# Optimization experiments

Measured on AMD Instinct MI355X. Metric: run time of the kernel, lower is better.

Reference implementation:

```python
import jax, jax.numpy as jnp
import numpy as np

N, NC, E, S = 65536, 24576, 524288, 256
VAR_DIM, H1, H2, H3, H4 = 6, 128, 128, 256, 128
THRE, EPS = 0.7, 1e-5


def _bn(x, g, b):
    # BatchNorm1d, training-mode batch statistics (biased var), dropout treated as identity
    mu = x.mean(0)
    v = x.var(0)
    return (x - mu) * jax.lax.rsqrt(v + EPS) * g + b


def _gcn_sparse(h, src, dst, ew, W, b):
    # PyG GCNConv with edge weights: add self-loops (weight 1), symmetric normalization
    n = h.shape[0]
    loop = jnp.arange(n)
    s = jnp.concatenate([src, loop])
    d = jnp.concatenate([dst, loop])
    w = jnp.concatenate([ew, jnp.ones((n,), h.dtype)])
    deg = jax.ops.segment_sum(w, d, num_segments=n)
    dinv = jnp.where(deg > 0, jax.lax.rsqrt(deg), 0.0)
    norm = dinv[s] * w * dinv[d]
    xw = h @ W.T  # [n, out]
    out = jax.ops.segment_sum(norm[:, None] * xw[s], d, num_segments=n)
    return out + b


def _gcn_dense(h, A, W, b):
    # GCNConv on a dense binary adjacency (no edge weights), self-loops + sym norm
    n = h.shape[0]
    A_hat = A + jnp.eye(n, dtype=h.dtype)
    deg = A_hat.sum(0)
    dinv = jnp.where(deg > 0, jax.lax.rsqrt(deg), 0.0)
    return dinv[:, None] * (A_hat.T @ ((h @ W.T) * dinv[:, None])) + b


def setup_inputs() -> dict:
    key = jax.random.key(0)
    ks = jax.random.split(key, 10)

    def w(k, o, i):
        return jax.random.normal(k, (o, i), jnp.float32) / np.float32(np.sqrt(i))

    x = jax.random.normal(ks[0], (N, VAR_DIM), jnp.float32)
    edge_attr = jax.random.uniform(ks[1], (E,), jnp.float32)
    scen_adj = jax.random.uniform(ks[2], (S, S), jnp.float32)
    edge_index = jax.random.randint(ks[3], (2, E), 0, N)
    batch = jnp.arange(N) // (N // S)  # sorted node->graph ids, 256 nodes per graph
    mark = jnp.concatenate([jnp.ones((NC,), jnp.int32), jnp.zeros((N - NC,), jnp.int32)])
    return {
        "x": x, "edge_attr": edge_attr, "scen_adj": scen_adj,
        "mlp_var_w": w(ks[4], H1, VAR_DIM), "mlp_var_b": jnp.zeros((H1,), jnp.float32),
        "mlp_con_w": w(ks[5], H1, 1), "mlp_con_b": jnp.zeros((H1,), jnp.float32),
        "conv1_w": w(ks[6], H2, H1), "conv1_b": jnp.zeros((H2,), jnp.float32),
        "conv2_w": w(ks[7], H3, H2), "conv2_b": jnp.zeros((H3,), jnp.float32),
        "conv3_w": w(ks[8], H4, H3), "conv3_b": jnp.zeros((H4,), jnp.float32),
        "bn1_g": jnp.ones((H1,), jnp.float32), "bn1_b": jnp.zeros((H1,), jnp.float32),
        "bn2_g": jnp.ones((H2,), jnp.float32), "bn2_b": jnp.zeros((H2,), jnp.float32),
        "bn3_g": jnp.ones((H3,), jnp.float32), "bn3_b": jnp.zeros((H3,), jnp.float32),
        "mark": mark, "edge_index": edge_index, "batch": batch, "n_con": NC,
    }


def reference(x, edge_attr, scen_adj, mlp_var_w, mlp_var_b, mlp_con_w, mlp_con_b,
              conv1_w, conv1_b, conv2_w, conv2_b, conv3_w, conv3_b,
              bn1_g, bn1_b, bn2_g, bn2_b, bn3_g, bn3_b,
              mark, edge_index, batch, n_con):
    nc = int(n_con)  # mark layout: first nc nodes are constraints (mark==1), rest vars
    con_feat = jnp.tanh(x[:nc, 0:1] @ mlp_con_w.T + mlp_con_b)
    var_feat = jnp.tanh(x[nc:] @ mlp_var_w.T + mlp_var_b)
    h = jnp.concatenate([con_feat, var_feat], axis=0)  # [N, H1], con-first as in torch cat
    h = _bn(h, bn1_g, bn1_b)  # dropout = identity (eval)
    h = _gcn_sparse(h, edge_index[0], edge_index[1], edge_attr, conv1_w, conv1_b)
    h = jnp.tanh(_bn(h, bn2_g, bn2_b))
    s = scen_adj.shape[0]
    sums = jax.ops.segment_sum(h, batch, num_segments=s)
    cnt = jax.ops.segment_sum(jnp.ones((h.shape[0],), h.dtype), batch, num_segments=s)
    pooled = sums / jnp.maximum(cnt, 1.0)[:, None]  # global_mean_pool -> [S, H2]
    A = (scen_adj >= THRE).astype(h.dtype)  # filter_adj + unweighted edges
    f = jnp.tanh(_bn(_gcn_dense(pooled, A, conv2_w, conv2_b), bn3_g, bn3_b))
    feat = jnp.tanh(_gcn_dense(f, A, conv3_w, conv3_b))
    return feat, feat.mean(0)
```

## Files before the change

kernel.cpp:

```cpp
#include <hip/hip_runtime.h>
#include <hip/hip_bf16.h>
#include <cstddef>

#define N_NODES 65536
#define N_EDGES 524288
#define S_GRAPH 256
#define BN_EPS 1e-5f
#define THRE 0.7f

typedef __hip_bfloat16 bf16;
typedef unsigned int uint32;
typedef unsigned char uchar;
typedef unsigned short ushort16;
typedef __attribute__((ext_vector_type(8))) short short8;
typedef __attribute__((ext_vector_type(4))) float f32x4;

__device__ __forceinline__ float blo(uint32 u) { return __uint_as_float(u << 16); }
__device__ __forceinline__ float bhi(uint32 u) { return __uint_as_float(u & 0xffff0000u); }

__device__ __forceinline__ uint32 packbf(float a, float b)
{
    bf16 ha = __float2bfloat16(a), hb = __float2bfloat16(b);
    unsigned short ua, ub;
    __builtin_memcpy(&ua, &ha, 2); __builtin_memcpy(&ub, &hb, 2);
    return (uint32)ua | ((uint32)ub << 16);
}

__device__ __forceinline__ float ftanh(float x)
{
    float e = __builtin_amdgcn_exp2f(x * 2.8853900817779268f);
    return 1.0f - 2.0f * __builtin_amdgcn_rcpf(e + 1.0f);
}

__global__ __launch_bounds__(256) void k_mlp_hist(
    const float* __restrict__ x, const float* __restrict__ wv,
    const float* __restrict__ bv, const float* __restrict__ wc,
    const float* __restrict__ bc, const int* __restrict__ nconp,
    uint32* __restrict__ h0u, float* __restrict__ stats,
    const int* __restrict__ dst, uint32* __restrict__ blkhist,
    const float* __restrict__ scen, float* __restrict__ fcol,
    const float* __restrict__ w1f, uint32* __restrict__ w1bk)
{
    __shared__ float xs[128 * 6];
    __shared__ float sh[256];
    __shared__ uint32 bh[256];
    int t = threadIdx.x;
    int b = blockIdx.x;
    if (b < 512) {
        bh[t] = 0;
        __syncthreads();
        int e0 = b * 1024 + t * 4;
        int4 d4 = *(const int4*)(dst + e0);
        atomicAdd(&bh[d4.x >> 8], 1u);
        atomicAdd(&bh[d4.y >> 8], 1u);
        atomicAdd(&bh[d4.z >> 8], 1u);
        atomicAdd(&bh[d4.w >> 8], 1u);
        __syncthreads();
        blkhist[b * 256 + t] = bh[t];
        return;
    }
    if (b >= 1024) {
        if (b < 1056) {
            int r0 = (b - 1024) * 8;
            float s = 0.f;
            for (int r = r0; r < r0 + 8; r++)
                s += (scen[r * 256 + t] >= THRE) ? 1.0f : 0.0f;
            atomicAdd(&fcol[t], s);
        } else {
            const float4* w4 = (const float4*)w1f;
            uint2* wo = (uint2*)w1bk;
            #pragma unroll
            for (int it = 0; it < 16; it++) {
                int fi = it * 256 + t;
                float4 w = w4[fi];
                wo[fi] = make_uint2(packbf(w.x, w.y), packbf(w.z, w.w));
            }
        }
        return;
    }
    int n0 = (b - 512) * 128;
    if (t < 192) ((float4*)xs)[t] = ((const float4*)(x + (size_t)n0 * 6))[t];
    __syncthreads();

    int nc = *nconp;
    int lane = t & 63, wave = t >> 6;
    int j0 = 2 * lane;
    const float2* wv2 = (const float2*)wv;
    float2 wa0 = wv2[j0 * 3], wa1 = wv2[j0 * 3 + 1], wa2 = wv2[j0 * 3 + 2];
    float2 wb0 = wv2[j0 * 3 + 3], wb1 = wv2[j0 * 3 + 4], wb2 = wv2[j0 * 3 + 5];
    float wc0 = wc[j0], wc1 = wc[j0 + 1], bc0 = bc[j0], bc1 = bc[j0 + 1];
    float bv0 = bv[j0], bv1 = bv[j0 + 1];

    float s0 = 0.f, ss0 = 0.f, s1 = 0.f, ss1 = 0.f;
    #pragma unroll 4
    for (int m = 0; m < 32; m++) {
        int ln = wave * 32 + m;
        int n = n0 + ln;
        const float* xr = &xs[ln * 6];
        float a0, a1;
        if (n < nc) {
            float xv = xr[0];
            a0 = xv * wc0 + bc0; a1 = xv * wc1 + bc1;
        } else {
            float x0 = xr[0], x1 = xr[1], x2 = xr[2], x3 = xr[3], x4 = xr[4], x5 = xr[5];
            a0 = bv0 + x0 * wa0.x + x1 * wa0.y + x2 * wa1.x + x3 * wa1.y + x4 * wa2.x + x5 * wa2.y;
            a1 = bv1 + x0 * wb0.x + x1 * wb0.y + x2 * wb1.x + x3 * wb1.y + x4 * wb2.x + x5 * wb2.y;
        }
        uint32 pk = packbf(ftanh(a0), ftanh(a1));
        h0u[(size_t)n * 64 + lane] = pk;
        float v0 = blo(pk), v1 = bhi(pk);
        s0 += v0; ss0 += v0 * v0; s1 += v1; ss1 += v1 * v1;
    }
    sh[t] = s0; __syncthreads();
    if (t < 64) atomicAdd(&stats[2 * t], sh[t] + sh[t + 64] + sh[t + 128] + sh[t + 192]);
    __syncthreads(); sh[t] = s1; __syncthreads();
    if (t < 64) atomicAdd(&stats[2 * t + 1], sh[t] + sh[t + 64] + sh[t + 128] + sh[t + 192]);
    __syncthreads(); sh[t] = ss0; __syncthreads();
    if (t < 64) atomicAdd(&stats[128 + 2 * t], sh[t] + sh[t + 64] + sh[t + 128] + sh[t + 192]);
    __syncthreads(); sh[t] = ss1; __syncthreads();
    if (t < 64) atomicAdd(&stats[128 + 2 * t + 1], sh[t] + sh[t + 64] + sh[t + 128] + sh[t + 192]);
}

__global__ __launch_bounds__(256) void k_binscan(
    const uint32* __restrict__ blkhist, uint32* __restrict__ blkoff,
    uint32* __restrict__ binsz, uint32* __restrict__ ubase,
    uint32* __restrict__ pbase, int* __restrict__ ctr)
{
    __shared__ uint32 v[512];
    __shared__ uint32 ps[256];
    __shared__ int flag;
    int g = blockIdx.x, t = threadIdx.x;
    v[t]       = blkhist[t * 256 + g];
    v[t + 256] = blkhist[(t + 256) * 256 + g];
    __syncthreads();
    uint32 a0 = v[2 * t], a1 = v[2 * t + 1];
    ps[t] = a0 + a1; __syncthreads();
    for (int o = 1; o < 256; o <<= 1) {
        uint32 u = (t >= o) ? ps[t - o] : 0;
        __syncthreads();
        ps[t] += u;
        __syncthreads();
    }
    uint32 ex = ps[t] - (a0 + a1);
    ((uint2*)blkoff)[g * 256 + t] = make_uint2(ex, ex + a0);
    if (t == 255) atomicExch((int*)&binsz[g], (int)ps[255]);
    __syncthreads();
    if (t == 0) {
        __threadfence();
        flag = (atomicAdd(ctr, 1) == 255) ? 1 : 0;
    }
    __syncthreads();
    if (flag) {
        __threadfence();
        uint32 s = binsz[t];
        ps[t] = s; __syncthreads();
        for (int o = 1; o < 256; o <<= 1) {
            uint32 u = (t >= o) ? ps[t - o] : 0;
            __syncthreads();
            ps[t] += u;
            __syncthreads();
        }
        ubase[t] = ps[t] - s;
        pbase[t] = ps[t] - s + (uint32)t * 768u;
    }
}

__global__ __launch_bounds__(256) void k_scatter(
    const int* __restrict__ src, const int* __restrict__ dst,
    const float* __restrict__ ew, const uint32* __restrict__ blkoff,
    const uint32* __restrict__ ubase, uint2* __restrict__ ebin)
{
    __shared__ uint32 bh[256];
    __shared__ uint32 bo[256];
    int b = blockIdx.x, t = threadIdx.x;
    bh[t] = 0;
    bo[t] = ubase[t] + blkoff[t * 512 + b];
    __syncthreads();
    int e0 = b * 1024 + t * 4;
    int4 d4 = *(const int4*)(dst + e0);
    int4 s4 = *(const int4*)(src + e0);
    float4 w4 = *(const float4*)(ew + e0);
    int bin; uint32 r;
    bin = d4.x >> 8; r = atomicAdd(&bh[bin], 1u);
    ebin[bo[bin] + r] = make_uint2((uint32)s4.x | ((uint32)(d4.x & 255) << 16), __float_as_uint(w4.x));
    bin = d4.y >> 8; r = atomicAdd(&bh[bin], 1u);
    ebin[bo[bin] + r] = make_uint2((uint32)s4.y | ((uint32)(d4.y & 255) << 16), __float_as_uint(w4.y));
    bin = d4.z >> 8; r = atomicAdd(&bh[bin], 1u);
    ebin[bo[bin] + r] = make_uint2((uint32)s4.z | ((uint32)(d4.z & 255) << 16), __float_as_uint(w4.z));
    bin = d4.w >> 8; r = atomicAdd(&bh[bin], 1u);
    ebin[bo[bin] + r] = make_uint2((uint32)s4.w | ((uint32)(d4.w & 255) << 16), __float_as_uint(w4.w));
}

__global__ __launch_bounds__(256) void k_csr(
    const uint2* __restrict__ ebin, const uint32* __restrict__ binsz,
    const uint32* __restrict__ ubase, const uint32* __restrict__ pbase,
    float* __restrict__ dinv, int* __restrict__ rowp, int* __restrict__ cnts,
    int2* __restrict__ epk)
{
    __shared__ uint2 es[3072];
    __shared__ uint32 hist[256];
    __shared__ int sscan[256];
    __shared__ int rloc[256];
    __shared__ float dlv[256];
    int g = blockIdx.x, t = threadIdx.x;
    int start = (int)ubase[g];
    int sz = min((int)binsz[g], 3072);
    int pb = (int)pbase[g];
    hist[t] = 0;
    __syncthreads();
    for (int i = t; i < sz; i += 256) {
        uint2 e = ebin[start + i];
        int dl = (e.x >> 16) & 255;
        uint32 wfix = __float2uint_rn(__uint_as_float(e.y) * 262144.0f);
        uint32 h = atomicAdd(&hist[dl], (1u << 24) | wfix);
        e.x |= (h >> 24) << 24;
        es[i] = e;
    }
    __syncthreads();
    uint32 hv = hist[t];
    int cnt = (int)(hv >> 24);
    float di = rsqrtf((float)(hv & 0xFFFFFFu) * 3.814697265625e-6f + 1.0f);
    dlv[t] = di;
    dinv[g * 256 + t] = di;
    cnts[g * 256 + t] = cnt;
    int pcnt = (cnt + 3) & ~3;
    sscan[t] = pcnt; __syncthreads();
    for (int o = 1; o < 256; o <<= 1) {
        int u = (t >= o) ? sscan[t - o] : 0;
        __syncthreads();
        sscan[t] += u;
        __syncthreads();
    }
    int rl = sscan[t] - pcnt;
    rloc[t] = rl;
    rowp[g * 256 + t] = pb + rl;
    __syncthreads();
    for (int i = t; i < sz; i += 256) {
        uint2 e = es[i];
        int s  = (int)(e.x & 0xFFFFu);
        int dl = (int)((e.x >> 16) & 255u);
        int r  = (int)(e.x >> 24);
        float w = __uint_as_float(e.y) * dlv[dl];
        epk[pb + rloc[dl] + r] = make_int2(s, __float_as_int(w));
    }
    int base = pb + rl;
    for (int q = cnt; q < pcnt; q++) epk[base + q] = make_int2(g * 256 + t, 0);
}

__global__ __launch_bounds__(256) void k_gemm1f(
    const uint32* __restrict__ h0u, const uint32* __restrict__ w1bk,
    const float* __restrict__ g1, const float* __restrict__ bb1,
    const float* __restrict__ stats, ushort16* __restrict__ xws,
    const float* __restrict__ dinv)
{
    __shared__ short hn_s[64 * 136];
    __shared__ short w_s[128 * 136];
    __shared__ float sc[128], sf[128];
    int t = threadIdx.x;
    int blk = blockIdx.x;
    int row0 = blk * 64;

    if (t < 128) {
        float mu  = stats[t] * (1.0f / N_NODES);
        float var = stats[128 + t] * (1.0f / N_NODES) - mu * mu;
        float rs  = rsqrtf(fmaxf(var, 0.f) + BN_EPS);
        float s   = rs * g1[t];
        sc[t] = s;
        sf[t] = bb1[t] - mu * s;
    }
    __syncthreads();

    const uint4* h4 = (const uint4*)(h0u + (size_t)row0 * 64);
    #pragma unroll
    for (int it = 0; it < 4; it++) {
        int slot = it * 256 + t;
        int r = slot >> 4, k0 = (slot & 15) * 8;
        uint4 u = h4[slot];
        uint32 ua[4] = {u.x, u.y, u.z, u.w};
        uint32 o[4];
        #pragma unroll
        for (int m = 0; m < 4; m++) {
            int k = k0 + 2 * m;
            o[m] = packbf(blo(ua[m]) * sc[k] + sf[k], bhi(ua[m]) * sc[k + 1] + sf[k + 1]);
        }
        *(uint4*)&hn_s[r * 136 + k0] = make_uint4(o[0], o[1], o[2], o[3]);
    }
    const uint4* wv4 = (const uint4*)w1bk;
    #pragma unroll
    for (int it = 0; it < 8; it++) {
        int s2 = it * 256 + t;
        int c = s2 >> 4, k0 = (s2 & 15) * 8;
        *(uint4*)&w_s[c * 136 + k0] = wv4[s2];
    }
    __syncthreads();

    int lane = t & 63, wave = t >> 6;
    int m16 = lane & 15, kh = lane >> 4;
    int mbase = wave * 16;
    f32x4 acc[8] = {};
    #pragma unroll
    for (int ks = 0; ks < 4; ks++) {
        short8 a = *(const short8*)&hn_s[(mbase + m16) * 136 + ks * 32 + kh * 8];
        #pragma unroll
        for (int ct = 0; ct < 8; ct++) {
            short8 bfr = *(const short8*)&w_s[(ct * 16 + m16) * 136 + ks * 32 + kh * 8];
            acc[ct] = __builtin_amdgcn_mfma_f32_16x16x32_bf16(a, bfr, acc[ct], 0, 0, 0);
        }
    }
    float dvr[4];
    #pragma unroll
    for (int r = 0; r < 4; r++) dvr[r] = dinv[row0 + mbase + kh * 4 + r];
    #pragma unroll
    for (int ct = 0; ct < 8; ct++) {
        int col = ct * 16 + m16;
        #pragma unroll
        for (int r = 0; r < 4; r++) {
            int row = mbase + kh * 4 + r;
            bf16 hv = __float2bfloat16(acc[ct][r] * dvr[r]);
            unsigned short us; __builtin_memcpy(&us, &hv, 2);
            xws[(size_t)(row0 + row) * 128 + col] = us;
        }
    }
}

__global__ __launch_bounds__(256) void k_gather(
    const int* __restrict__ rowp, const int* __restrict__ cnts,
    const int2* __restrict__ epk, const uint32* __restrict__ xwu,
    const float* __restrict__ dinv, const float2* __restrict__ b1c2,
    uint32* __restrict__ aggu, float* __restrict__ stats2r)
{
    __shared__ float sh[256];
    int t = threadIdx.x, b = blockIdx.x;
    int lane = t & 63, wave = t >> 6;
    float2 bb = b1c2[lane];
    float s0 = 0.f, ss0 = 0.f, s1 = 0.f, ss1 = 0.f;
    for (int it = 0; it < 8; it++) {
        int n = b * 32 + it * 4 + wave;
        int st = rowp[n];
        int pcnt = (cnts[n] + 3) & ~3;
        float di = dinv[n];
        uint32 u0 = xwu[(size_t)n * 64 + lane];
        float ax = di * blo(u0) + bb.x;
        float ay = di * bhi(u0) + bb.y;
        int en = st + pcnt;
        for (int p = st; p < en; p += 4) {
            int2 q0 = epk[p], q1 = epk[p + 1], q2 = epk[p + 2], q3 = epk[p + 3];
            uint32 v0 = xwu[(size_t)q0.x * 64 + lane];
            uint32 v1 = xwu[(size_t)q1.x * 64 + lane];
            uint32 v2 = xwu[(size_t)q2.x * 64 + lane];
            uint32 v3 = xwu[(size_t)q3.x * 64 + lane];
            float w0 = __int_as_float(q0.y), w1 = __int_as_float(q1.y);
            float w2 = __int_as_float(q2.y), w3 = __int_as_float(q3.y);
            ax += w0 * blo(v0) + w1 * blo(v1) + w2 * blo(v2) + w3 * blo(v3);
            ay += w0 * bhi(v0) + w1 * bhi(v1) + w2 * bhi(v2) + w3 * bhi(v3);
        }
        uint32 pk = packbf(ax, ay);
        aggu[(size_t)n * 64 + lane] = pk;
        float v0 = blo(pk), v1 = bhi(pk);
        s0 += v0; ss0 += v0 * v0; s1 += v1; ss1 += v1 * v1;
    }
    float* st2 = stats2r + (b & 7) * 256;
    sh[t] = s0; __syncthreads();
    if (t < 64) atomicAdd(&st2[2 * t], sh[t] + sh[t + 64] + sh[t + 128] + sh[t + 192]);
    __syncthreads(); sh[t] = s1; __syncthreads();
    if (t < 64) atomicAdd(&st2[2 * t + 1], sh[t] + sh[t + 64] + sh[t + 128] + sh[t + 192]);
    __syncthreads(); sh[t] = ss0; __syncthreads();
    if (t < 64) atomicAdd(&st2[128 + 2 * t], sh[t] + sh[t + 64] + sh[t + 128] + sh[t + 192]);
    __syncthreads(); sh[t] = ss1; __syncthreads();
    if (t < 64) atomicAdd(&st2[128 + 2 * t + 1], sh[t] + sh[t + 64] + sh[t + 128] + sh[t + 192]);
}

__global__ __launch_bounds__(512) void k_poolg2(
    const uint32* __restrict__ aggu, const float* __restrict__ stats2r,
    const float* __restrict__ g2, const float* __restrict__ bb2,
    const float* __restrict__ w2, float* __restrict__ z1)
{
    __shared__ float sc[128], sf[128], sh[512], prow[128];
    int t = threadIdx.x, g = blockIdx.x;
    if (t < 128) {
        float su = 0.f, sq = 0.f;
        #pragma unroll
        for (int r = 0; r < 8; r++) {
            su += stats2r[r * 256 + t];
            sq += stats2r[r * 256 + 128 + t];
        }
        float mu  = su * (1.0f / N_NODES);
        float var = sq * (1.0f / N_NODES) - mu * mu;
        float rs  = rsqrtf(fmaxf(var, 0.f) + BN_EPS);
        float s   = rs * g2[t];
        sc[t] = s;
        sf[t] = bb2[t] - mu * s;
    }
    __syncthreads();
    int c = t & 63, grp = t >> 6;
    float c0s = sc[2 * c], c0f = sf[2 * c], c1s = sc[2 * c + 1], c1f = sf[2 * c + 1];
    const uint32* base = aggu + (size_t)g * 256 * 64;
    float s0 = 0.f, s1 = 0.f;
    for (int r = grp * 32; r < grp * 32 + 32; r++) {
        uint32 u = base[r * 64 + c];
        s0 += ftanh(blo(u) * c0s + c0f);
        s1 += ftanh(bhi(u) * c1s + c1f);
    }
    sh[t] = s0; __syncthreads();
    if (t < 64) {
        float acc = 0.f;
        #pragma unroll
        for (int k = 0; k < 8; k++) acc += sh[t + 64 * k];
        prow[2 * t] = acc * (1.0f / 256.0f);
    }
    __syncthreads(); sh[t] = s1; __syncthreads();
    if (t < 64) {
        float acc = 0.f;
        #pragma unroll
        for (int k = 0; k < 8; k++) acc += sh[t + 64 * k];
        prow[2 * t + 1] = acc * (1.0f / 256.0f);
    }
    __syncthreads();
    if (t < 256) {
        float acc = 0.f;
        const float* wr = w2 + t * 128;
        for (int k = 0; k < 128; k++) acc += prow[k] * wr[k];
        z1[g * 256 + t] = acc;
    }
}

__global__ void k_dgcn1(const float* __restrict__ scen, const float* __restrict__ fcol,
                        const float* __restrict__ z1, const float* __restrict__ b2c,
                        float* __restrict__ y1, float* __restrict__ stats3r)
{
    __shared__ float wk[256];
    int i = blockIdx.x, t = threadIdx.x;
    float a = (scen[t * 256 + i] >= THRE) ? 1.0f : 0.0f;
    if (t == i) a += 1.0f;
    wk[t] = a * rsqrtf(fcol[t] + 1.0f);
    __syncthreads();
    float acc = 0.f;
    for (int k = 0; k < 256; k++) acc += wk[k] * z1[k * 256 + t];
    float v = rsqrtf(fcol[i] + 1.0f) * acc + b2c[t];
    y1[i * 256 + t] = v;
    float* s3 = stats3r + (i & 7) * 512;
    atomicAdd(&s3[t], v);
    atomicAdd(&s3[256 + t], v * v);
}

__global__ void k_gemm3(const float* __restrict__ y1, const float* __restrict__ stats3r,
                        const float* __restrict__ g3, const float* __restrict__ bb3,
                        const float* __restrict__ w3, float* __restrict__ z2)
{
    __shared__ float row[256];
    int i = blockIdx.x, t = threadIdx.x;
    for (int c = t; c < 256; c += 128) {
        float s = 0.f, ss = 0.f;
        #pragma unroll
        for (int r = 0; r < 8; r++) {
            s  += stats3r[r * 512 + c];
            ss += stats3r[r * 512 + 256 + c];
        }
        float mu  = s * (1.0f / 256.0f);
        float var = ss * (1.0f / 256.0f) - mu * mu;
        float rs  = rsqrtf(fmaxf(var, 0.f) + BN_EPS);
        float scj = rs * g3[c];
        float sfj = bb3[c] - mu * scj;
        row[c] = ftanh(y1[i * 256 + c] * scj + sfj);
    }
    __syncthreads();
    float acc = 0.f;
    const float* wr = w3 + t * 256;
    for (int k = 0; k < 256; k++) acc += row[k] * wr[k];
    z2[i * 128 + t] = acc;
}

__global__ void k_dgcn2(const float* __restrict__ scen, const float* __restrict__ fcol,
                        const float* __restrict__ z2, const float* __restrict__ b3c,
                        float* __restrict__ out, float* __restrict__ meanr,
                        int* __restrict__ ctr)
{
    __shared__ float wk[256];
    __shared__ int flag;
    int i = blockIdx.x, t = threadIdx.x;
    for (int k = t; k < 256; k += 128) {
        float a = (scen[k * 256 + i] >= THRE) ? 1.0f : 0.0f;
        if (k == i) a += 1.0f;
        wk[k] = a * rsqrtf(fcol[k] + 1.0f);
    }
    __syncthreads();
    float acc = 0.f;
    for (int k = 0; k < 256; k++) acc += wk[k] * z2[k * 128 + t];
    float v = ftanh(rsqrtf(fcol[i] + 1.0f) * acc + b3c[t]);
    out[i * 128 + t] = v;
    atomicAdd(&meanr[(i & 7) * 128 + t], v);
    __syncthreads();
    if (t == 0) {
        __threadfence();
        flag = (atomicAdd(ctr, 1) == 255) ? 1 : 0;
    }
    __syncthreads();
    if (flag) {
        __threadfence();
        float s = 0.f;
        #pragma unroll
        for (int r = 0; r < 8; r++) s += meanr[r * 128 + t];
        out[S_GRAPH * 128 + t] = s * (1.0f / 256.0f);
    }
}

extern "C" void kernel_launch(void* const* d_in, const int* in_sizes, int n_in,
                              void* d_out, int out_size, void* d_ws, size_t ws_size,
                              hipStream_t stream)
{
    const float* x        = (const float*)d_in[0];
    const float* edge_attr= (const float*)d_in[1];
    const float* scen     = (const float*)d_in[2];
    const float* wv       = (const float*)d_in[3];
    const float* bv       = (const float*)d_in[4];
    const float* wc       = (const float*)d_in[5];
    const float* bc       = (const float*)d_in[6];
    const float* w1       = (const float*)d_in[7];
    const float* b1c      = (const float*)d_in[8];
    const float* w2       = (const float*)d_in[9];
    const float* b2c      = (const float*)d_in[10];
    const float* w3       = (const float*)d_in[11];
    const float* b3c      = (const float*)d_in[12];
    const float* g1       = (const float*)d_in[13];
    const float* bb1      = (const float*)d_in[14];
    const float* g2       = (const float*)d_in[15];
    const float* bb2      = (const float*)d_in[16];
    const float* g3       = (const float*)d_in[17];
    const float* bb3      = (const float*)d_in[18];
    const int*  ei        = (const int*)d_in[20];
    const int*  nconp     = (const int*)d_in[22];
    const int*  src = ei;
    const int*  dst = ei + N_EDGES;

    float* wsf = (float*)d_ws;
    uint32*   h0u  = (uint32*)wsf;
    uint32*   aggu = (uint32*)wsf;
    uint32*   xwu  = (uint32*)(wsf + 4194304);
    float* zb      = wsf + 8388608;
    float* stats1  = zb;
    float* stats2r = zb + 512;
    float* stats3r = zb + 2560;
    float* fcol    = zb + 6656;
    float* meanr   = zb + 6912;
    int*   ctrs    = (int*)(zb + 7936);
    const int ZN   = 7944;
    float* deg     = zb + ZN;
    int*   rowp    = (int*)(deg + 65536);
    int*   cnts    = rowp + 65536;
    uint32* blkhist= (uint32*)(cnts + 65536);
    uint32* blkoff = blkhist + 131072;
    uint32* binsz  = blkoff + 131072;
    uint32* ubase  = binsz + 256;
    uint32* pbase  = ubase + 256;
    uint2* ebin    = (uint2*)(pbase + 256);
    int2*  epk     = (int2*)(ebin + 524288);
    uint32* w1bk   = (uint32*)(epk + 720896);
    float* z1      = (float*)(w1bk + 8192);
    float* y1      = z1 + 65536;
    float* z2      = y1 + 65536;

    float* out = (float*)d_out;

    hipMemsetAsync(zb, 0, ZN * sizeof(float), stream);

    k_mlp_hist<<<1057, 256, 0, stream>>>(x, wv, bv, wc, bc, nconp, h0u, stats1,
                                         dst, blkhist, scen, fcol, w1, w1bk);
    k_binscan<<<256, 256, 0, stream>>>(blkhist, blkoff, binsz, ubase, pbase, &ctrs[0]);
    k_scatter<<<512, 256, 0, stream>>>(src, dst, edge_attr, blkoff, ubase, ebin);
    k_csr<<<256, 256, 0, stream>>>(ebin, binsz, ubase, pbase, deg, rowp, cnts, epk);
    k_gemm1f<<<1024, 256, 0, stream>>>(h0u, w1bk, g1, bb1, stats1, (ushort16*)xwu, deg);
    k_gather<<<2048, 256, 0, stream>>>(rowp, cnts, epk, xwu, deg,
                                       (const float2*)b1c, aggu, stats2r);
    k_poolg2<<<S_GRAPH, 512, 0, stream>>>(aggu, stats2r, g2, bb2, w2, z1);
    k_dgcn1<<<256, 256, 0, stream>>>(scen, fcol, z1, b2c, y1, stats3r);
    k_gemm3<<<256, 128, 0, stream>>>(y1, stats3r, g3, bb3, w3, z2);
    k_dgcn2<<<256, 128, 0, stream>>>(scen, fcol, z2, b3c, out, meanr, &ctrs[1]);
}
```

Measured before the change: 253.3 us.

## Fuse front-end and tail kernels into persistent kernels with grid barriers

Merges the MLP/histogram, bin scan, scatter and CSR-build kernels into one 1057-block kernel separated by software grid barriers. It also merges the four small dense-GCN tail kernels into one 256-block kernel. The aim is to remove kernel launch gaps and drain/ramp overhead between many short dependent stages. The cost is that the grid barriers require every block to be co-resident, which is why launch bounds were raised to 5 blocks per CU. Barrier spin and a larger shared-memory footprint could also reduce occupancy.

```diff
diff --git a/kernel.cpp b/kernel.cpp
--- a/kernel.cpp
+++ b/kernel.cpp
@@ -32,21 +32,43 @@
     return 1.0f - 2.0f * __builtin_amdgcn_rcpf(e + 1.0f);
 }
 
-__global__ __launch_bounds__(256) void k_mlp_hist(
+__device__ __forceinline__ void gbar(int* bar, int nblk)
+{
+    __syncthreads();
+    if (threadIdx.x == 0) {
+        __builtin_amdgcn_fence(__ATOMIC_RELEASE, "agent");
+        int gen = __hip_atomic_load(bar + 1, __ATOMIC_RELAXED, __HIP_MEMORY_SCOPE_AGENT);
+        if (__hip_atomic_fetch_add(bar, 1, __ATOMIC_RELAXED, __HIP_MEMORY_SCOPE_AGENT) == nblk - 1) {
+            __hip_atomic_store(bar, 0, __ATOMIC_RELAXED, __HIP_MEMORY_SCOPE_AGENT);
+            __hip_atomic_fetch_add(bar + 1, 1, __ATOMIC_RELAXED, __HIP_MEMORY_SCOPE_AGENT);
+        } else {
+            while (__hip_atomic_load(bar + 1, __ATOMIC_RELAXED, __HIP_MEMORY_SCOPE_AGENT) == gen)
+                __builtin_amdgcn_s_sleep(8);
+        }
+        __builtin_amdgcn_fence(__ATOMIC_ACQUIRE, "agent");
+    }
+    __syncthreads();
+}
+
+__global__ __launch_bounds__(256, 5) void k_front(
     const float* __restrict__ x, const float* __restrict__ wv,
     const float* __restrict__ bv, const float* __restrict__ wc,
     const float* __restrict__ bc, const int* __restrict__ nconp,
     uint32* __restrict__ h0u, float* __restrict__ stats,
-    const int* __restrict__ dst, uint32* __restrict__ blkhist,
+    const int* __restrict__ src, const int* __restrict__ dst,
+    const float* __restrict__ ew, uint32* __restrict__ blkhist,
+    uint32* __restrict__ blkoff, uint32* __restrict__ binsz,
     const float* __restrict__ scen, float* __restrict__ fcol,
-    const float* __restrict__ w1f, uint32* __restrict__ w1bk)
-{
-    __shared__ float xs[128 * 6];
-    __shared__ float sh[256];
-    __shared__ uint32 bh[256];
+    const float* __restrict__ w1f, uint32* __restrict__ w1bk,
+    float* __restrict__ dinv, int* __restrict__ rowp, int* __restrict__ cnts,
+    uint2* __restrict__ ebin, int2* __restrict__ epk, int* __restrict__ bar)
+{
+    __shared__ __align__(16) uchar smem[29696];
     int t = threadIdx.x;
     int b = blockIdx.x;
+
     if (b < 512) {
+        uint32* bh = (uint32*)smem;
         bh[t] = 0;
         __syncthreads();
         int e0 = b * 1024 + t * 4;
@@ -57,101 +79,93 @@
         atomicAdd(&bh[d4.w >> 8], 1u);
         __syncthreads();
         blkhist[b * 256 + t] = bh[t];
-        return;
-    }
-    if (b >= 1024) {
-        if (b < 1056) {
-            int r0 = (b - 1024) * 8;
-            float s = 0.f;
-            for (int r = r0; r < r0 + 8; r++)
-                s += (scen[r * 256 + t] >= THRE) ? 1.0f : 0.0f;
-            atomicAdd(&fcol[t], s);
-        } else {
-            const float4* w4 = (const float4*)w1f;
-            uint2* wo = (uint2*)w1bk;
-            #pragma unroll
-            for (int it = 0; it < 16; it++) {
-                int fi = it * 256 + t;
-                float4 w = w4[fi];
-                wo[fi] = make_uint2(packbf(w.x, w.y), packbf(w.z, w.w));
+    } else if (b < 1024) {
+        float* xs = (float*)smem;
+        float* sh = (float*)(smem + 3072);
+        int n0 = (b - 512) * 128;
+        if (t < 192) ((float4*)xs)[t] = ((const float4*)(x + (size_t)n0 * 6))[t];
+        __syncthreads();
+
+        int nc = *nconp;
+        int lane = t & 63, wave = t >> 6;
+        int j0 = 2 * lane;
+        const float2* wv2 = (const float2*)wv;
+        float2 wa0 = wv2[j0 * 3], wa1 = wv2[j0 * 3 + 1], wa2 = wv2[j0 * 3 + 2];
+        float2 wb0 = wv2[j0 * 3 + 3], wb1 = wv2[j0 * 3 + 4], wb2 = wv2[j0 * 3 + 5];
+        float wc0 = wc[j0], wc1 = wc[j0 + 1], bc0 = bc[j0], bc1 = bc[j0 + 1];
+        float bv0 = bv[j0], bv1 = bv[j0 + 1];
+
+        float s0 = 0.f, ss0 = 0.f, s1 = 0.f, ss1 = 0.f;
+        #pragma unroll 4
+        for (int m = 0; m < 32; m++) {
+            int ln = wave * 32 + m;
+            int n = n0 + ln;
+            const float* xr = &xs[ln * 6];
+            float a0, a1;
+            if (n < nc) {
+                float xv = xr[0];
+                a0 = xv * wc0 + bc0; a1 = xv * wc1 + bc1;
+            } else {
+                float x0 = xr[0], x1 = xr[1], x2 = xr[2], x3 = xr[3], x4 = xr[4], x5 = xr[5];
+                a0 = bv0 + x0 * wa0.x + x1 * wa0.y + x2 * wa1.x + x3 * wa1.y + x4 * wa2.x + x5 * wa2.y;
+                a1 = bv1 + x0 * wb0.x + x1 * wb0.y + x2 * wb1.x + x3 * wb1.y + x4 * wb2.x + x5 * wb2.y;
             }
-        }
-        return;
-    }
-    int n0 = (b - 512) * 128;
-    if (t < 192) ((float4*)xs)[t] = ((const float4*)(x + (size_t)n0 * 6))[t];
-    __syncthreads();
-
-    int nc = *nconp;
-    int lane = t & 63, wave = t >> 6;
-    int j0 = 2 * lane;
-    const float2* wv2 = (const float2*)wv;
-    float2 wa0 = wv2[j0 * 3], wa1 = wv2[j0 * 3 + 1], wa2 = wv2[j0 * 3 + 2];
-    float2 wb0 = wv2[j0 * 3 + 3], wb1 = wv2[j0 * 3 + 4], wb2 = wv2[j0 * 3 + 5];
-    float wc0 = wc[j0], wc1 = wc[j0 + 1], bc0 = bc[j0], bc1 = bc[j0 + 1];
-    float bv0 = bv[j0], bv1 = bv[j0 + 1];
-
-    float s0 = 0.f, ss0 = 0.f, s1 = 0.f, ss1 = 0.f;
-    #pragma unroll 4
-    for (int m = 0; m < 32; m++) {
-        int ln = wave * 32 + m;
-        int n = n0 + ln;
-        const float* xr = &xs[ln * 6];
-        float a0, a1;
-        if (n < nc) {
-            float xv = xr[0];
-            a0 = xv * wc0 + bc0; a1 = xv * wc1 + bc1;
-        } else {
-            float x0 = xr[0], x1 = xr[1], x2 = xr[2], x3 = xr[3], x4 = xr[4], x5 = xr[5];
-            a0 = bv0 + x0 * wa0.x + x1 * wa0.y + x2 * wa1.x + x3 * wa1.y + x4 * wa2.x + x5 * wa2.y;
-            a1 = bv1 + x0 * wb0.x + x1 * wb0.y + x2 * wb1.x + x3 * wb1.y + x4 * wb2.x + x5 * wb2.y;
-        }
-        uint32 pk = packbf(ftanh(a0), ftanh(a1));
-        h0u[(size_t)n * 64 + lane] = pk;
-        float v0 = blo(pk), v1 = bhi(pk);
-        s0 += v0; ss0 += v0 * v0; s1 += v1; ss1 += v1 * v1;
-    }
-    sh[t] = s0; __syncthreads();
-    if (t < 64) atomicAdd(&stats[2 * t], sh[t] + sh[t + 64] + sh[t + 128] + sh[t + 192]);
-    __syncthreads(); sh[t] = s1; __syncthreads();
-    if (t < 64) atomicAdd(&stats[2 * t + 1], sh[t] + sh[t + 64] + sh[t + 128] + sh[t + 192]);
-    __syncthreads(); sh[t] = ss0; __syncthreads();
-    if (t < 64) atomicAdd(&stats[128 + 2 * t], sh[t] + sh[t + 64] + sh[t + 128] + sh[t + 192]);
-    __syncthreads(); sh[t] = ss1; __syncthreads();
-    if (t < 64) atomicAdd(&stats[128 + 2 * t + 1], sh[t] + sh[t + 64] + sh[t + 128] + sh[t + 192]);
-}
-
-__global__ __launch_bounds__(256) void k_binscan(
-    const uint32* __restrict__ blkhist, uint32* __restrict__ blkoff,
-    uint32* __restrict__ binsz, uint32* __restrict__ ubase,
-    uint32* __restrict__ pbase, int* __restrict__ ctr)
-{
-    __shared__ uint32 v[512];
-    __shared__ uint32 ps[256];
-    __shared__ int flag;
-    int g = blockIdx.x, t = threadIdx.x;
-    v[t]       = blkhist[t * 256 + g];
-    v[t + 256] = blkhist[(t + 256) * 256 + g];
-    __syncthreads();
-    uint32 a0 = v[2 * t], a1 = v[2 * t + 1];
-    ps[t] = a0 + a1; __syncthreads();
-    for (int o = 1; o < 256; o <<= 1) {
-        uint32 u = (t >= o) ? ps[t - o] : 0;
-        __syncthreads();
-        ps[t] += u;
-        __syncthreads();
-    }
-    uint32 ex = ps[t] - (a0 + a1);
-    ((uint2*)blkoff)[g * 256 + t] = make_uint2(ex, ex + a0);
-    if (t == 255) atomicExch((int*)&binsz[g], (int)ps[255]);
-    __syncthreads();
-    if (t == 0) {
-        __threadfence();
-        flag = (atomicAdd(ctr, 1) == 255) ? 1 : 0;
-    }
-    __syncthreads();
-    if (flag) {
-        __threadfence();
+            uint32 pk = packbf(ftanh(a0), ftanh(a1));
+            h0u[(size_t)n * 64 + lane] = pk;
+            float v0 = blo(pk), v1 = bhi(pk);
+            s0 += v0; ss0 += v0 * v0; s1 += v1; ss1 += v1 * v1;
+        }
+        sh[t] = s0; __syncthreads();
+        if (t < 64) atomicAdd(&stats[2 * t], sh[t] + sh[t + 64] + sh[t + 128] + sh[t + 192]);
+        __syncthreads(); sh[t] = s1; __syncthreads();
+        if (t < 64) atomicAdd(&stats[2 * t + 1], sh[t] + sh[t + 64] + sh[t + 128] + sh[t + 192]);
+        __syncthreads(); sh[t] = ss0; __syncthreads();
+        if (t < 64) atomicAdd(&stats[128 + 2 * t], sh[t] + sh[t + 64] + sh[t + 128] + sh[t + 192]);
+        __syncthreads(); sh[t] = ss1; __syncthreads();
+        if (t < 64) atomicAdd(&stats[128 + 2 * t + 1], sh[t] + sh[t + 64] + sh[t + 128] + sh[t + 192]);
+    } else if (b < 1056) {
+        int r0 = (b - 1024) * 8;
+        float s = 0.f;
+        for (int r = r0; r < r0 + 8; r++)
+            s += (scen[r * 256 + t] >= THRE) ? 1.0f : 0.0f;
+        atomicAdd(&fcol[t], s);
+    } else {
+        const float4* w4 = (const float4*)w1f;
+        uint2* wo = (uint2*)w1bk;
+        #pragma unroll
+        for (int it = 0; it < 16; it++) {
+            int fi = it * 256 + t;
+            float4 w = w4[fi];
+            wo[fi] = make_uint2(packbf(w.x, w.y), packbf(w.z, w.w));
+        }
+    }
+    gbar(bar, 1057);
+
+    if (b < 256) {
+        uint32* v  = (uint32*)smem;
+        uint32* ps = (uint32*)(smem + 2048);
+        int g = b;
+        v[t]       = blkhist[t * 256 + g];
+        v[t + 256] = blkhist[(t + 256) * 256 + g];
+        __syncthreads();
+        uint32 a0 = v[2 * t], a1 = v[2 * t + 1];
+        ps[t] = a0 + a1; __syncthreads();
+        for (int o = 1; o < 256; o <<= 1) {
+            uint32 u = (t >= o) ? ps[t - o] : 0;
+            __syncthreads();
+            ps[t] += u;
+            __syncthreads();
+        }
+        uint32 ex = ps[t] - (a0 + a1);
+        ((uint2*)blkoff)[g * 256 + t] = make_uint2(ex, ex + a0);
+        if (t == 255) binsz[g] = ps[255];
+    }
+    gbar(bar, 1057);
+
+    if (b < 512) {
+        uint32* ps = (uint32*)smem;
+        uint32* bo = (uint32*)(smem + 1024);
+        uint32* bh = (uint32*)(smem + 2048);
         uint32 s = binsz[t];
         ps[t] = s; __syncthreads();
         for (int o = 1; o < 256; o <<= 1) {
@@ -160,91 +174,88 @@
             ps[t] += u;
             __syncthreads();
         }
-        ubase[t] = ps[t] - s;
-        pbase[t] = ps[t] - s + (uint32)t * 768u;
-    }
-}
-
-__global__ __launch_bounds__(256) void k_scatter(
-    const int* __restrict__ src, const int* __restrict__ dst,
-    const float* __restrict__ ew, const uint32* __restrict__ blkoff,
-    const uint32* __restrict__ ubase, uint2* __restrict__ ebin)
-{
-    __shared__ uint32 bh[256];
-    __shared__ uint32 bo[256];
-    int b = blockIdx.x, t = threadIdx.x;
-    bh[t] = 0;
-    bo[t] = ubase[t] + blkoff[t * 512 + b];
-    __syncthreads();
-    int e0 = b * 1024 + t * 4;
-    int4 d4 = *(const int4*)(dst + e0);
-    int4 s4 = *(const int4*)(src + e0);
-    float4 w4 = *(const float4*)(ew + e0);
-    int bin; uint32 r;
-    bin = d4.x >> 8; r = atomicAdd(&bh[bin], 1u);
-    ebin[bo[bin] + r] = make_uint2((uint32)s4.x | ((uint32)(d4.x & 255) << 16), __float_as_uint(w4.x));
-    bin = d4.y >> 8; r = atomicAdd(&bh[bin], 1u);
-    ebin[bo[bin] + r] = make_uint2((uint32)s4.y | ((uint32)(d4.y & 255) << 16), __float_as_uint(w4.y));
-    bin = d4.z >> 8; r = atomicAdd(&bh[bin], 1u);
-    ebin[bo[bin] + r] = make_uint2((uint32)s4.z | ((uint32)(d4.z & 255) << 16), __float_as_uint(w4.z));
-    bin = d4.w >> 8; r = atomicAdd(&bh[bin], 1u);
-    ebin[bo[bin] + r] = make_uint2((uint32)s4.w | ((uint32)(d4.w & 255) << 16), __float_as_uint(w4.w));
-}
-
-__global__ __launch_bounds__(256) void k_csr(
-    const uint2* __restrict__ ebin, const uint32* __restrict__ binsz,
-    const uint32* __restrict__ ubase, const uint32* __restrict__ pbase,
-    float* __restrict__ dinv, int* __restrict__ rowp, int* __restrict__ cnts,
-    int2* __restrict__ epk)
-{
-    __shared__ uint2 es[3072];
-    __shared__ uint32 hist[256];
-    __shared__ int sscan[256];
-    __shared__ int rloc[256];
-    __shared__ float dlv[256];
-    int g = blockIdx.x, t = threadIdx.x;
-    int start = (int)ubase[g];
-    int sz = min((int)binsz[g], 3072);
-    int pb = (int)pbase[g];
-    hist[t] = 0;
-    __syncthreads();
-    for (int i = t; i < sz; i += 256) {
-        uint2 e = ebin[start + i];
-        int dl = (e.x >> 16) & 255;
-        uint32 wfix = __float2uint_rn(__uint_as_float(e.y) * 262144.0f);
-        uint32 h = atomicAdd(&hist[dl], (1u << 24) | wfix);
-        e.x |= (h >> 24) << 24;
-        es[i] = e;
-    }
-    __syncthreads();
-    uint32 hv = hist[t];
-    int cnt = (int)(hv >> 24);
-    float di = rsqrtf((float)(hv & 0xFFFFFFu) * 3.814697265625e-6f + 1.0f);
-    dlv[t] = di;
-    dinv[g * 256 + t] = di;
-    cnts[g * 256 + t] = cnt;
-    int pcnt = (cnt + 3) & ~3;
-    sscan[t] = pcnt; __syncthreads();
-    for (int o = 1; o < 256; o <<= 1) {
-        int u = (t >= o) ? sscan[t - o] : 0;
-        __syncthreads();
-        sscan[t] += u;
-        __syncthreads();
-    }
-    int rl = sscan[t] - pcnt;
-    rloc[t] = rl;
-    rowp[g * 256 + t] = pb + rl;
-    __syncthreads();
-    for (int i = t; i < sz; i += 256) {
-        uint2 e = es[i];
-        int s  = (int)(e.x & 0xFFFFu);
-        int dl = (int)((e.x >> 16) & 255u);
-        int r  = (int)(e.x >> 24);
-        float w = __uint_as_float(e.y) * dlv[dl];
-        epk[pb + rloc[dl] + r] = make_int2(s, __float_as_int(w));
-    }
-    int base = pb + rl;
-    for (int q = cnt; q < pcnt; q++) epk[base + q] = make_int2(g * 256 + t, 0);
+        bo[t] = (ps[t] - s) + blkoff[t * 512 + b];
+        bh[t] = 0;
+        __syncthreads();
+        int e0 = b * 1024 + t * 4;
+        int4 d4 = *(const int4*)(dst + e0);
+        int4 s4 = *(const int4*)(src + e0);
+        float4 w4 = *(const float4*)(ew + e0);
+        int bin; uint32 r;
+        bin = d4.x >> 8; r = atomicAdd(&bh[bin], 1u);
+        ebin[bo[bin] + r] = make_uint2((uint32)s4.x | ((uint32)(d4.x & 255) << 16), __float_as_uint(w4.x));
+        bin = d4.y >> 8; r = atomicAdd(&bh[bin], 1u);
+        ebin[bo[bin] + r] = make_uint2((uint32)s4.y | ((uint32)(d4.y & 255) << 16), __float_as_uint(w4.y));
+        bin = d4.z >> 8; r = atomicAdd(&bh[bin], 1u);
+        ebin[bo[bin] + r] = make_uint2((uint32)s4.z | ((uint32)(d4.z & 255) << 16), __float_as_uint(w4.z));
+        bin = d4.w >> 8; r = atomicAdd(&bh[bin], 1u);
+        ebin[bo[bin] + r] = make_uint2((uint32)s4.w | ((uint32)(d4.w & 255) << 16), __float_as_uint(w4.w));
+    }
+    gbar(bar, 1057);
+
+    if (b < 256) {
+        uint2* es    = (uint2*)smem;
+        uint32* hist = (uint32*)(smem + 24576);
+        int* sscan   = (int*)(smem + 25600);
+        int* rloc    = (int*)(smem + 26624);
+        float* dlv   = (float*)(smem + 27648);
+        uint32* ubl  = (uint32*)(smem + 28672);
+        int g = b;
+        {
+            uint32 s = binsz[t];
+            sscan[t] = (int)s; __syncthreads();
+            for (int o = 1; o < 256; o <<= 1) {
+                int u = (t >= o) ? sscan[t - o] : 0;
+                __syncthreads();
+                sscan[t] += u;
+                __syncthreads();
+            }
+            ubl[t] = (uint32)sscan[t] - s;
+        }
+        __syncthreads();
+        int start = (int)ubl[g];
+        int sz = min((int)binsz[g], 3072);
+        int pb = start + g * 768;
+        hist[t] = 0;
+        __syncthreads();
+        for (int i2 = t; i2 < sz; i2 += 256) {
+            uint2 e = ebin[start + i2];
+            int dl = (e.x >> 16) & 255;
+            uint32 wfix = __float2uint_rn(__uint_as_float(e.y) * 262144.0f);
+            uint32 h = atomicAdd(&hist[dl], (1u << 24) | wfix);
+            e.x |= (h >> 24) << 24;
+            es[i2] = e;
+        }
+        __syncthreads();
+        uint32 hv = hist[t];
+        int cnt = (int)(hv >> 24);
+        float di = rsqrtf((float)(hv & 0xFFFFFFu) * 3.814697265625e-6f + 1.0f);
+        dlv[t] = di;
+        dinv[g * 256 + t] = di;
+        cnts[g * 256 + t] = cnt;
+        int pcnt = (cnt + 3) & ~3;
+        sscan[t] = pcnt; __syncthreads();
+        for (int o = 1; o < 256; o <<= 1) {
+            int u = (t >= o) ? sscan[t - o] : 0;
+            __syncthreads();
+            sscan[t] += u;
+            __syncthreads();
+        }
+        int rl = sscan[t] - pcnt;
+        rloc[t] = rl;
+        rowp[g * 256 + t] = pb + rl;
+        __syncthreads();
+        for (int i2 = t; i2 < sz; i2 += 256) {
+            uint2 e = es[i2];
+            int s2 = (int)(e.x & 0xFFFFu);
+            int dl = (int)((e.x >> 16) & 255u);
+            int r  = (int)(e.x >> 24);
+            float w = __uint_as_float(e.y) * dlv[dl];
+            epk[pb + rloc[dl] + r] = make_int2(s2, __float_as_int(w));
+        }
+        int basep = pb + rl;
+        for (int q = cnt; q < pcnt; q++) epk[basep + q] = make_int2(g * 256 + t, 0);
+    }
 }
 
 __global__ __launch_bounds__(256) void k_gemm1f(
@@ -370,137 +381,146 @@
     if (t < 64) atomicAdd(&st2[128 + 2 * t + 1], sh[t] + sh[t + 64] + sh[t + 128] + sh[t + 192]);
 }
 
-__global__ __launch_bounds__(512) void k_poolg2(
+__global__ __launch_bounds__(256) void k_tail(
     const uint32* __restrict__ aggu, const float* __restrict__ stats2r,
     const float* __restrict__ g2, const float* __restrict__ bb2,
-    const float* __restrict__ w2, float* __restrict__ z1)
-{
-    __shared__ float sc[128], sf[128], sh[512], prow[128];
-    int t = threadIdx.x, g = blockIdx.x;
-    if (t < 128) {
-        float su = 0.f, sq = 0.f;
-        #pragma unroll
-        for (int r = 0; r < 8; r++) {
-            su += stats2r[r * 256 + t];
-            sq += stats2r[r * 256 + 128 + t];
-        }
-        float mu  = su * (1.0f / N_NODES);
-        float var = sq * (1.0f / N_NODES) - mu * mu;
-        float rs  = rsqrtf(fmaxf(var, 0.f) + BN_EPS);
-        float s   = rs * g2[t];
-        sc[t] = s;
-        sf[t] = bb2[t] - mu * s;
-    }
-    __syncthreads();
-    int c = t & 63, grp = t >> 6;
-    float c0s = sc[2 * c], c0f = sf[2 * c], c1s = sc[2 * c + 1], c1f = sf[2 * c + 1];
-    const uint32* base = aggu + (size_t)g * 256 * 64;
-    float s0 = 0.f, s1 = 0.f;
-    for (int r = grp * 32; r < grp * 32 + 32; r++) {
-        uint32 u = base[r * 64 + c];
-        s0 += ftanh(blo(u) * c0s + c0f);
-        s1 += ftanh(bhi(u) * c1s + c1f);
-    }
-    sh[t] = s0; __syncthreads();
-    if (t < 64) {
+    const float* __restrict__ w2, float* __restrict__ z1,
+    const float* __restrict__ scen, const float* __restrict__ fcol,
+    const float* __restrict__ b2c, float* __restrict__ y1,
+    float* __restrict__ stats3r, const float* __restrict__ g3,
+    const float* __restrict__ bb3, const float* __restrict__ w3,
+    float* __restrict__ z2, const float* __restrict__ b3c,
+    float* __restrict__ out, float* __restrict__ meanr,
+    int* __restrict__ ctr, int* __restrict__ bar)
+{
+    __shared__ __align__(16) uchar smem[2560];
+    __shared__ int flagP10;
+    int t = threadIdx.x;
+    int b = blockIdx.x;
+
+    {
+        float* sc   = (float*)smem;
+        float* sf   = (float*)(smem + 512);
+        float* sh   = (float*)(smem + 1024);
+        float* prow = (float*)(smem + 2048);
+        int g = b;
+        if (t < 128) {
+            float su = 0.f, sq = 0.f;
+            #pragma unroll
+            for (int r = 0; r < 8; r++) {
+                su += stats2r[r * 256 + t];
+                sq += stats2r[r * 256 + 128 + t];
+            }
+            float mu  = su * (1.0f / N_NODES);
+            float var = sq * (1.0f / N_NODES) - mu * mu;
+            float rs  = rsqrtf(fmaxf(var, 0.f) + BN_EPS);
+            float s   = rs * g2[t];
+            sc[t] = s;
+            sf[t] = bb2[t] - mu * s;
+        }
+        __syncthreads();
+        int c = t & 63, grp = t >> 6;
+        float c0s = sc[2 * c], c0f = sf[2 * c], c1s = sc[2 * c + 1], c1f = sf[2 * c + 1];
+        const uint32* base = aggu + (size_t)g * 256 * 64;
+        float s0 = 0.f, s1 = 0.f;
+        for (int r = grp * 64; r < grp * 64 + 64; r++) {
+            uint32 u = base[r * 64 + c];
+            s0 += ftanh(blo(u) * c0s + c0f);
+            s1 += ftanh(bhi(u) * c1s + c1f);
+        }
+        sh[t] = s0; __syncthreads();
+        if (t < 64) {
+            float acc = sh[t] + sh[t + 64] + sh[t + 128] + sh[t + 192];
+            prow[2 * t] = acc * (1.0f / 256.0f);
+        }
+        __syncthreads(); sh[t] = s1; __syncthreads();
+        if (t < 64) {
+            float acc = sh[t] + sh[t + 64] + sh[t + 128] + sh[t + 192];
+            prow[2 * t + 1] = acc * (1.0f / 256.0f);
+        }
+        __syncthreads();
+        float accv = 0.f;
+        const float* wr = w2 + t * 128;
+        for (int k = 0; k < 128; k++) accv += prow[k] * wr[k];
+        z1[g * 256 + t] = accv;
+    }
+    gbar(bar, 256);
+
+    {
+        float* wk = (float*)smem;
+        int i = b;
+        float aa = (scen[t * 256 + i] >= THRE) ? 1.0f : 0.0f;
+        if (t == i) aa += 1.0f;
+        wk[t] = aa * rsqrtf(fcol[t] + 1.0f);
+        __syncthreads();
         float acc = 0.f;
-        #pragma unroll
-        for (int k = 0; k < 8; k++) acc += sh[t + 64 * k];
-        prow[2 * t] = acc * (1.0f / 256.0f);
-    }
-    __syncthreads(); sh[t] = s1; __syncthreads();
-    if (t < 64) {
-        float acc = 0.f;
-        #pragma unroll
-        for (int k = 0; k < 8; k++) acc += sh[t + 64 * k];
-        prow[2 * t + 1] = acc * (1.0f / 256.0f);
-    }
-    __syncthreads();
-    if (t < 256) {
-        float acc = 0.f;
-        const float* wr = w2 + t * 128;
-        for (int k = 0; k < 128; k++) acc += prow[k] * wr[k];
-        z1[g * 256 + t] = acc;
-    }
-}
-
-__global__ void k_dgcn1(const float* __restrict__ scen, const float* __restrict__ fcol,
-                        const float* __restrict__ z1, const float* __restrict__ b2c,
-                        float* __restrict__ y1, float* __restrict__ stats3r)
-{
-    __shared__ float wk[256];
-    int i = blockIdx.x, t = threadIdx.x;
-    float a = (scen[t * 256 + i] >= THRE) ? 1.0f : 0.0f;
-    if (t == i) a += 1.0f;
-    wk[t] = a * rsqrtf(fcol[t] + 1.0f);
-    __syncthreads();
-    float acc = 0.f;
-    for (int k = 0; k < 256; k++) acc += wk[k] * z1[k * 256 + t];
-    float v = rsqrtf(fcol[i] + 1.0f) * acc + b2c[t];
-    y1[i * 256 + t] = v;
-    float* s3 = stats3r + (i & 7) * 512;
-    atomicAdd(&s3[t], v);
-    atomicAdd(&s3[256 + t], v * v);
-}
-
-__global__ void k_gemm3(const float* __restrict__ y1, const float* __restrict__ stats3r,
-                        const float* __restrict__ g3, const float* __restrict__ bb3,
-                        const float* __restrict__ w3, float* __restrict__ z2)
-{
-    __shared__ float row[256];
-    int i = blockIdx.x, t = threadIdx.x;
-    for (int c = t; c < 256; c += 128) {
-        float s = 0.f, ss = 0.f;
-        #pragma unroll
-        for (int r = 0; r < 8; r++) {
-            s  += stats3r[r * 512 + c];
-            ss += stats3r[r * 512 + 256 + c];
-        }
-        float mu  = s * (1.0f / 256.0f);
-        float var = ss * (1.0f / 256.0f) - mu * mu;
-        float rs  = rsqrtf(fmaxf(var, 0.f) + BN_EPS);
-        float scj = rs * g3[c];
-        float sfj = bb3[c] - mu * scj;
-        row[c] = ftanh(y1[i * 256 + c] * scj + sfj);
-    }
-    __syncthreads();
-    float acc = 0.f;
-    const float* wr = w3 + t * 256;
-    for (int k = 0; k < 256; k++) acc += row[k] * wr[k];
-    z2[i * 128 + t] = acc;
-}
-
-__global__ void k_dgcn2(const float* __restrict__ scen, const float* __restrict__ fcol,
-                        const float* __restrict__ z2, const float* __restrict__ b3c,
-                        float* __restrict__ out, float* __restrict__ meanr,
-                        int* __restrict__ ctr)
-{
-    __shared__ float wk[256];
-    __shared__ int flag;
-    int i = blockIdx.x, t = threadIdx.x;
-    for (int k = t; k < 256; k += 128) {
-        float a = (scen[k * 256 + i] >= THRE) ? 1.0f : 0.0f;
-        if (k == i) a += 1.0f;
-        wk[k] = a * rsqrtf(fcol[k] + 1.0f);
-    }
-    __syncthreads();
-    float acc = 0.f;
-    for (int k = 0; k < 256; k++) acc += wk[k] * z2[k * 128 + t];
-    float v = ftanh(rsqrtf(fcol[i] + 1.0f) * acc + b3c[t]);
-    out[i * 128 + t] = v;
-    atomicAdd(&meanr[(i & 7) * 128 + t], v);
-    __syncthreads();
-    if (t == 0) {
-        __threadfence();
-        flag = (atomicAdd(ctr, 1) == 255) ? 1 : 0;
-    }
-    __syncthreads();
-    if (flag) {
-        __threadfence();
-        float s = 0.f;
-        #pragma unroll
-        for (int r = 0; r < 8; r++) s += meanr[r * 128 + t];
-        out[S_GRAPH * 128 + t] = s * (1.0f / 256.0f);
+        for (int k = 0; k < 256; k++) acc += wk[k] * z1[k * 256 + t];
+        float v = rsqrtf(fcol[i] + 1.0f) * acc + b2c[t];
+        y1[i * 256 + t] = v;
+        float* s3 = stats3r + (i & 7) * 512;
+        atomicAdd(&s3[t], v);
+        atomicAdd(&s3[256 + t], v * v);
+    }
+    gbar(bar, 256);
+
+    {
+        float* row = (float*)smem;
+        int i = b;
+        {
+            float s = 0.f, ss = 0.f;
+            #pragma unroll
+            for (int r = 0; r < 8; r++) {
+                s  += stats3r[r * 512 + t];
+                ss += stats3r[r * 512 + 256 + t];
+            }
+            float mu  = s * (1.0f / 256.0f);
+            float var = ss * (1.0f / 256.0f) - mu * mu;
+            float rs  = rsqrtf(fmaxf(var, 0.f) + BN_EPS);
+            float scj = rs * g3[t];
+            float sfj = bb3[t] - mu * scj;
+            row[t] = ftanh(y1[i * 256 + t] * scj + sfj);
+        }
+        __syncthreads();
+        if (t < 128) {
+            float acc = 0.f;
+            const float* wr = w3 + t * 256;
+            for (int k = 0; k < 256; k++) acc += row[k] * wr[k];
+            z2[i * 128 + t] = acc;
+        }
+    }
+    gbar(bar, 256);
+
+    {
+        float* wk = (float*)smem;
+        int i = b;
+        {
+            float aa = (scen[t * 256 + i] >= THRE) ? 1.0f : 0.0f;
+            if (t == i) aa += 1.0f;
+            wk[t] = aa * rsqrtf(fcol[t] + 1.0f);
+        }
+        __syncthreads();
+        if (t < 128) {
+            float acc = 0.f;
+            for (int k = 0; k < 256; k++) acc += wk[k] * z2[k * 128 + t];
+            float v = ftanh(rsqrtf(fcol[i] + 1.0f) * acc + b3c[t]);
+            out[i * 128 + t] = v;
+            atomicAdd(&meanr[(i & 7) * 128 + t], v);
+        }
+        __syncthreads();
+        if (t == 0) {
+            __threadfence();
+            flagP10 = (atomicAdd(ctr, 1) == 255) ? 1 : 0;
+        }
+        __syncthreads();
+        if (flagP10) {
+            __threadfence();
+            if (t < 128) {
+                float s = 0.f;
+                #pragma unroll
+                for (int r = 0; r < 8; r++) s += meanr[r * 128 + t];
+                out[S_GRAPH * 128 + t] = s * (1.0f / 256.0f);
+            }
+        }
     }
 }
 
@@ -550,9 +570,7 @@
     uint32* blkhist= (uint32*)(cnts + 65536);
     uint32* blkoff = blkhist + 131072;
     uint32* binsz  = blkoff + 131072;
-    uint32* ubase  = binsz + 256;
-    uint32* pbase  = ubase + 256;
-    uint2* ebin    = (uint2*)(pbase + 256);
+    uint2* ebin    = (uint2*)(binsz + 256 + 512);
     int2*  epk     = (int2*)(ebin + 524288);
     uint32* w1bk   = (uint32*)(epk + 720896);
     float* z1      = (float*)(w1bk + 8192);
@@ -563,16 +581,15 @@
 
     hipMemsetAsync(zb, 0, ZN * sizeof(float), stream);
 
-    k_mlp_hist<<<1057, 256, 0, stream>>>(x, wv, bv, wc, bc, nconp, h0u, stats1,
-                                         dst, blkhist, scen, fcol, w1, w1bk);
-    k_binscan<<<256, 256, 0, stream>>>(blkhist, blkoff, binsz, ubase, pbase, &ctrs[0]);
-    k_scatter<<<512, 256, 0, stream>>>(src, dst, edge_attr, blkoff, ubase, ebin);
-    k_csr<<<256, 256, 0, stream>>>(ebin, binsz, ubase, pbase, deg, rowp, cnts, epk);
+    k_front<<<1057, 256, 0, stream>>>(x, wv, bv, wc, bc, nconp, h0u, stats1,
+                                      src, dst, edge_attr, blkhist, blkoff,
+                                      binsz, scen, fcol, w1, w1bk,
+                                      deg, rowp, cnts, ebin, epk, &ctrs[2]);
     k_gemm1f<<<1024, 256, 0, stream>>>(h0u, w1bk, g1, bb1, stats1, (ushort16*)xwu, deg);
     k_gather<<<2048, 256, 0, stream>>>(rowp, cnts, epk, xwu, deg,
                                        (const float2*)b1c, aggu, stats2r);
-    k_poolg2<<<S_GRAPH, 512, 0, stream>>>(aggu, stats2r, g2, bb2, w2, z1);
-    k_dgcn1<<<256, 256, 0, stream>>>(scen, fcol, z1, b2c, y1, stats3r);
-    k_gemm3<<<256, 128, 0, stream>>>(y1, stats3r, g3, bb3, w3, z2);
-    k_dgcn2<<<256, 128, 0, stream>>>(scen, fcol, z2, b3c, out, meanr, &ctrs[1]);
-}
+    k_tail<<<256, 256, 0, stream>>>(aggu, stats2r, g2, bb2, w2, z1,
+                                    scen, fcol, b2c, y1, stats3r,
+                                    g3, bb3, w3, z2, b3c, out, meanr,
+                                    &ctrs[1], &ctrs[4]);
+}
```

After: 552.6 us. 2.18x slower.
